# Performance work log

Hardware: AMD Instinct MI355X
Metric: run time of the kernel (lower is better)

The kernel has to match this reference:

```python
import jax, jax.numpy as jnp
import numpy as np

N, E, IN, H, D = 50000, 800000, 128, 2, 64  # heads=2, head_dim=64, hidden*2 = 128


def setup_inputs() -> dict:
    key = jax.random.key(0)
    ks = jax.random.split(key, 8)
    s = 1.0 / np.sqrt(IN)
    return {
        "x": jax.random.normal(ks[0], (N, IN), dtype=jnp.float32),
        "edge_index": jax.random.randint(ks[1], (2, E), 0, N, dtype=jnp.int64),
        "Wq": jax.random.normal(ks[2], (IN, H * D), dtype=jnp.float32) * s,
        "bq": jnp.zeros((H * D,), jnp.float32),
        "Wk": jax.random.normal(ks[3], (IN, H * D), dtype=jnp.float32) * s,
        "bk": jnp.zeros((H * D,), jnp.float32),
        "Wv": jax.random.normal(ks[4], (IN, H * D), dtype=jnp.float32) * s,
        "bv": jnp.zeros((H * D,), jnp.float32),
        "Wskip": jax.random.normal(ks[5], (IN, H * D), dtype=jnp.float32) * s,
        "bskip": jnp.zeros((H * D,), jnp.float32),
        "Wdec": jax.random.normal(ks[6], (H * D, IN), dtype=jnp.float32) * (1.0 / np.sqrt(H * D)),
        "bdec": jnp.zeros((IN,), jnp.float32),
    }


def reference(x, edge_index, Wq, bq, Wk, bk, Wv, bv, Wskip, bskip, Wdec, bdec):
    n = x.shape[0]
    src, dst = edge_index[0], edge_index[1]  # message flows src -> dst (PyG convention)
    q = (x @ Wq + bq).reshape(n, H, D)
    k = (x @ Wk + bk).reshape(n, H, D)
    v = (x @ Wv + bv).reshape(n, H, D)
    # per-edge multi-head scores [E, H]
    score = jnp.einsum('ehd,ehd->eh', q[dst], k[src]) / jnp.sqrt(jnp.asarray(D, x.dtype))
    # segment softmax over in-edges of each destination node
    m = jax.ops.segment_max(score, dst, num_segments=n)
    m = jnp.where(jnp.isfinite(m), m, jnp.zeros_like(m))  # nodes with no in-edges
    e = jnp.exp(score - m[dst])
    denom = jax.ops.segment_sum(e, dst, num_segments=n) + 1e-16
    alpha = e / denom[dst]                      # [E, H]
    msg = v[src] * alpha[..., None]             # [E, H, D]
    agg = jax.ops.segment_sum(msg, dst, num_segments=n)  # [N, H, D]
    z = agg.reshape(n, H * D) + (x @ Wskip + bskip)       # concat heads + root skip
    x_hat = z @ Wdec + bdec
    return (x_hat, z)
```

## Files before the change

### kernel.cpp

```cpp
#include <hip/hip_runtime.h>
#include <hip/hip_bf16.h>
#include <math.h>

typedef unsigned short u16;
typedef unsigned char u8;
typedef unsigned int u32;
typedef __attribute__((ext_vector_type(8))) short bf16x8;
typedef __attribute__((ext_vector_type(4))) float f32x4;

__device__ __forceinline__ float b2f(u16 u) {
  union { unsigned int i; float f; } x; x.i = ((unsigned int)u) << 16; return x.f;
}
__device__ __forceinline__ u16 f2b(float f) {
  union { float f; unsigned int i; } x; x.f = f;
  unsigned int r = x.i + 0x7FFFu + ((x.i >> 16) & 1u);
  return (u16)(r >> 16);
}
__device__ __forceinline__ float4 cvt4(ushort4 u) {
  return make_float4(b2f(u.x), b2f(u.y), b2f(u.z), b2f(u.w));
}
__device__ __forceinline__ float4 i8x4_to_f4(u32 w) {
  return make_float4((float)((int)(w << 24) >> 24), (float)((int)(w << 16) >> 24),
                     (float)((int)(w << 8) >> 24), (float)((int)w >> 24));
}

#if __has_builtin(__builtin_amdgcn_sdot4)
__device__ __forceinline__ int dot4i8(u32 a, u32 b) {
  return __builtin_amdgcn_sdot4((int)a, (int)b, 0, false);
}
#else
__device__ __forceinline__ int dot4i8(u32 a, u32 b) {
  int s = ((int)(a << 24) >> 24) * ((int)(b << 24) >> 24);
  s += ((int)(a << 16) >> 24) * ((int)(b << 16) >> 24);
  s += ((int)(a << 8) >> 24) * ((int)(b << 8) >> 24);
  s += ((int)a >> 24) * ((int)b >> 24);
  return s;
}
#endif

__device__ __forceinline__ bool ei_is_i64(const int* __restrict__ ei) {
  return (ei[1] | ei[3] | ei[5] | ei[7] | ei[9] | ei[11] | ei[13] | ei[15]) == 0;
}

__global__ __launch_bounds__(256) void prep_kernel(
    const float* __restrict__ Wq, const float* __restrict__ Wk,
    const float* __restrict__ Wv, const float* __restrict__ Wsk,
    const float* __restrict__ Wd,
    const float* __restrict__ bq, const float* __restrict__ bk,
    const float* __restrict__ bv, const float* __restrict__ bsk,
    const float* __restrict__ bd,
    short* __restrict__ Wt, float* __restrict__ bias,
    const int* __restrict__ ei, int* __restrict__ cnt,
    u8* __restrict__ rank, int E) {
  int g = blockIdx.x * 256 + threadIdx.x;
  if (g < 5 * 16384) {
    int mat = g >> 14, rem = g & 16383;
    int frag = rem >> 9;
    int l = (rem >> 3) & 63;
    int j = rem & 7;
    int nt = frag >> 2, s = frag & 3;
    int nrow = nt * 16 + (l & 15);
    int kcol = s * 32 + (l >> 4) * 8 + j;
    const float* W = (mat == 0) ? Wq : (mat == 1) ? Wk : (mat == 2) ? Wv
                     : (mat == 3) ? Wsk : Wd;
    float scl = (mat == 0) ? 0.125f : 1.f;
    Wt[g] = (short)f2b(W[kcol * 128 + nrow] * scl);
  }
  if (g < 5 * 128) {
    int mat = g >> 7, nn = g & 127;
    const float* B = (mat == 0) ? bq : (mat == 1) ? bk : (mat == 2) ? bv
                     : (mat == 3) ? bsk : bd;
    bias[g] = B[nn] * ((mat == 0) ? 0.125f : 1.f);
  }
  bool f = ei_is_i64(ei);
  if (g < E) {
    int idx = f ? (g << 1) : g;
    int dbase = f ? (E << 1) : E;
    int d = ei[dbase + idx];
    rank[g] = (u8)atomicAdd(&cnt[d], 1);
  }
}

__global__ __launch_bounds__(1024) void scanA_kernel(const int* __restrict__ cnt,
                                                     int* __restrict__ offs,
                                                     int* __restrict__ parts, int n) {
  __shared__ int wsum[16];
  int i = blockIdx.x * 1024 + threadIdx.x;
  int lane = threadIdx.x & 63, wid = threadIdx.x >> 6;
  int v = (i < n) ? cnt[i] : 0;
  int s = v;
#pragma unroll
  for (int off = 1; off < 64; off <<= 1) {
    int t = __shfl_up(s, off, 64);
    if (lane >= off) s += t;
  }
  if (lane == 63) wsum[wid] = s;
  __syncthreads();
  if (threadIdx.x == 0) {
    int acc = 0;
#pragma unroll
    for (int w = 0; w < 16; ++w) { int t = wsum[w]; wsum[w] = acc; acc += t; }
    parts[blockIdx.x] = acc;
  }
  __syncthreads();
  if (i < n) offs[i] = wsum[wid] + (s - v);
}

__global__ __launch_bounds__(1024) void scanC_kernel(int* __restrict__ offs,
                                                     const int* __restrict__ parts,
                                                     int n, int nb) {
  __shared__ int sh[2];
  if (threadIdx.x < 64) {
    int lane = threadIdx.x;
    int v = (lane < nb) ? parts[lane] : 0;
    int s = v;
#pragma unroll
    for (int off = 1; off < 64; off <<= 1) {
      int t = __shfl_up(s, off, 64);
      if (lane >= off) s += t;
    }
    int base = __shfl(s - v, blockIdx.x, 64);
    int tot  = __shfl(s, nb - 1, 64);
    if (lane == 0) { sh[0] = base; sh[1] = tot; }
  }
  __syncthreads();
  int i = blockIdx.x * 1024 + threadIdx.x;
  if (i < n) offs[i] += sh[0];
  if (i == 0) offs[n] = sh[1];
}

__global__ __launch_bounds__(512) void proj_kernel(const float* __restrict__ x,
    const short* __restrict__ Wt, const float* __restrict__ bias,
    u32* __restrict__ q8, float* __restrict__ qscb,
    u32* __restrict__ kvq, float* __restrict__ scb,
    u32* __restrict__ skip32, int n,
    const int* __restrict__ ei, const int* __restrict__ offs,
    const u8* __restrict__ rank, int* __restrict__ csr, int E) {
  __shared__ short xt[32 * 128];
  __shared__ u32 qsL[32 * 33];
  __shared__ u32 kvL[32 * 65];
  __shared__ u32 skL[32 * 65];
  __shared__ float qscL[32 * 2];
  __shared__ float scL[32 * 4];
  int m0 = blockIdx.x * 32;
  int tid = threadIdx.x;

  {
    int row = tid >> 4, c = tid & 15;
    int grow = m0 + row;
    bf16x8 val;
    if (grow < n) {
      const float* sp = x + (size_t)grow * 128 + c * 8;
      float4 f0 = *(const float4*)sp;
      float4 f1 = *(const float4*)(sp + 4);
      val[0] = (short)f2b(f0.x); val[1] = (short)f2b(f0.y);
      val[2] = (short)f2b(f0.z); val[3] = (short)f2b(f0.w);
      val[4] = (short)f2b(f1.x); val[5] = (short)f2b(f1.y);
      val[6] = (short)f2b(f1.z); val[7] = (short)f2b(f1.w);
    } else {
#pragma unroll
      for (int j = 0; j < 8; ++j) val[j] = 0;
    }
    *(bf16x8*)&xt[row * 128 + ((c ^ (row & 15)) << 3)] = val;
  }
  __syncthreads();

  int wid = tid >> 6, l = tid & 63;
  int mat = wid & 3, mhalf = wid >> 2;
  int lm = l & 15, lk = l >> 4;
  const short* Wl = Wt + (size_t)mat * 16384 + l * 8;
  int ml = mhalf * 16 + lm;
  f32x4 acc[8];
#pragma unroll
  for (int nt = 0; nt < 8; ++nt) acc[nt] = (f32x4){0.f, 0.f, 0.f, 0.f};

#pragma unroll
  for (int s = 0; s < 4; ++s) {
    int c = s * 4 + lk;
    bf16x8 bfrag = *(const bf16x8*)&xt[ml * 128 + ((c ^ (ml & 15)) << 3)];
#pragma unroll
    for (int nt = 0; nt < 8; ++nt) {
      bf16x8 afrag = *(const bf16x8*)(Wl + nt * 2048 + s * 512);
      acc[nt] = __builtin_amdgcn_mfma_f32_16x16x32_bf16(afrag, bfrag, acc[nt], 0, 0, 0);
    }
  }

  const float* bs = bias + mat * 128;
#pragma unroll
  for (int nt = 0; nt < 8; ++nt) {
    float4 b4 = *(const float4*)(bs + nt * 16 + lk * 4);
    acc[nt][0] += b4.x; acc[nt][1] += b4.y;
    acc[nt][2] += b4.z; acc[nt][3] += b4.w;
  }
  int lrow = mhalf * 16 + lm;
  if (mat < 3) {
#pragma unroll
    for (int h = 0; h < 2; ++h) {
      float am = 0.f;
#pragma unroll
      for (int nt4 = 0; nt4 < 4; ++nt4) {
        int nt = h * 4 + nt4;
#pragma unroll
        for (int j = 0; j < 4; ++j) am = fmaxf(am, fabsf(acc[nt][j]));
      }
      am = fmaxf(am, __shfl_xor(am, 16));
      am = fmaxf(am, __shfl_xor(am, 32));
      float inv = (am > 0.f) ? 127.f / am : 0.f;
#pragma unroll
      for (int nt4 = 0; nt4 < 4; ++nt4) {
        int nt = h * 4 + nt4;
        u32 pk = 0;
#pragma unroll
        for (int j = 0; j < 4; ++j) {
          float qv = fminf(fmaxf(rintf(acc[nt][j] * inv), -127.f), 127.f);
          pk |= ((u32)((int)qv & 0xff)) << (8 * j);
        }
        int slot = nt4 * 4 + lk;
        if (mat == 0) qsL[lrow * 33 + h * 16 + slot] = pk;
        else kvL[lrow * 65 + h * 32 + slot * 2 + (mat - 1)] = pk;
      }
      if (lk == 0) {
        float sc = am * (1.f / 127.f);
        if (mat == 0) qscL[lrow * 2 + h] = sc;
        else scL[lrow * 4 + h * 2 + (mat - 1)] = sc;
      }
    }
  } else {
#pragma unroll
    for (int nt = 0; nt < 8; ++nt) {
      u16 o0 = f2b(acc[nt][0]), o1 = f2b(acc[nt][1]);
      u16 o2 = f2b(acc[nt][2]), o3 = f2b(acc[nt][3]);
      int u = nt * 8 + lk * 2;
      skL[lrow * 65 + u]     = (u32)o0 | ((u32)o1 << 16);
      skL[lrow * 65 + u + 1] = (u32)o2 | ((u32)o3 << 16);
    }
  }
  __syncthreads();

  int nvalid = n - m0; if (nvalid > 32) nvalid = 32;
  for (int idx = tid; idx < nvalid * 32; idx += 512) {
    int node = idx >> 5, slot = idx & 31;
    q8[(size_t)(m0 + node) * 32 + slot] = qsL[node * 33 + slot];
  }
  for (int idx = tid; idx < nvalid * 64; idx += 512) {
    int node = idx >> 6, slot = idx & 63;
    kvq[(size_t)(m0 + node) * 64 + slot] = kvL[node * 65 + slot];
  }
  for (int idx = tid; idx < nvalid * 64; idx += 512) {
    int node = idx >> 6, slot = idx & 63;
    skip32[(size_t)(m0 + node) * 64 + slot] = skL[node * 65 + slot];
  }
  for (int idx = tid; idx < nvalid * 4; idx += 512) {
    int node = idx >> 2, s = idx & 3;
    scb[(size_t)(m0 + node) * 4 + s] = scL[node * 4 + s];
  }
  for (int idx = tid; idx < nvalid * 2; idx += 512) {
    int node = idx >> 1, h = idx & 1;
    qscb[(size_t)(m0 + node) * 2 + h] = qscL[node * 2 + h];
  }

  {
    bool f = ei_is_i64(ei);
    int stride = gridDim.x * 512;
    for (int e = blockIdx.x * 512 + tid; e < E; e += stride) {
      int idx = f ? (e << 1) : e;
      int dbase = f ? (E << 1) : E;
      int s = ei[idx];
      int d = ei[dbase + idx];
      int pos = offs[d] + (int)rank[e];
      __builtin_nontemporal_store(s, &csr[pos]);
    }
  }
}

__global__ __launch_bounds__(256) void dec_kernel(const float* __restrict__ zin,
    const short* __restrict__ Wt, const float* __restrict__ bias,
    float* __restrict__ out, int n) {
  __shared__ short zt[128 * 128];
  int m0 = blockIdx.x * 128;
  int tid = threadIdx.x;
#pragma unroll
  for (int p = 0; p < 8; ++p) {
    int cid = tid + p * 256;
    int row = cid >> 4, c = cid & 15;
    int grow = m0 + row;
    bf16x8 val;
    if (grow < n) {
      const float* sp = zin + (size_t)grow * 128 + c * 8;
      float4 f0 = *(const float4*)sp;
      float4 f1 = *(const float4*)(sp + 4);
      val[0] = (short)f2b(f0.x); val[1] = (short)f2b(f0.y);
      val[2] = (short)f2b(f0.z); val[3] = (short)f2b(f0.w);
      val[4] = (short)f2b(f1.x); val[5] = (short)f2b(f1.y);
      val[6] = (short)f2b(f1.z); val[7] = (short)f2b(f1.w);
    } else {
#pragma unroll
      for (int j = 0; j < 8; ++j) val[j] = 0;
    }
    *(bf16x8*)&zt[row * 128 + ((c ^ (row & 15)) << 3)] = val;
  }
  __syncthreads();

  int wid = tid >> 6, l = tid & 63;
  int lm = l & 15, lk = l >> 4;
  int mbase = wid * 32;
  const short* Wl = Wt + l * 8;
  f32x4 acc[2][8];
#pragma unroll
  for (int mt = 0; mt < 2; ++mt)
#pragma unroll
    for (int nt = 0; nt < 8; ++nt) acc[mt][nt] = (f32x4){0.f, 0.f, 0.f, 0.f};

#pragma unroll
  for (int s = 0; s < 4; ++s) {
    bf16x8 bfrag[2];
#pragma unroll
    for (int mt = 0; mt < 2; ++mt) {
      int ml = mbase + mt * 16 + lm;
      int c = s * 4 + lk;
      bfrag[mt] = *(const bf16x8*)&zt[ml * 128 + ((c ^ (ml & 15)) << 3)];
    }
#pragma unroll
    for (int nt = 0; nt < 8; ++nt) {
      bf16x8 afrag = *(const bf16x8*)(Wl + nt * 2048 + s * 512);
      acc[0][nt] = __builtin_amdgcn_mfma_f32_16x16x32_bf16(afrag, bfrag[0], acc[0][nt], 0, 0, 0);
      acc[1][nt] = __builtin_amdgcn_mfma_f32_16x16x32_bf16(afrag, bfrag[1], acc[1][nt], 0, 0, 0);
    }
  }

#pragma unroll
  for (int mt = 0; mt < 2; ++mt) {
    int m = m0 + mbase + mt * 16 + lm;
    if (m >= n) continue;
#pragma unroll
    for (int nt = 0; nt < 8; ++nt) {
      int n4 = nt * 16 + lk * 4;
      float4 b4 = *(const float4*)(bias + n4);
      f32x4 a = acc[mt][nt];
      *(float4*)(out + (size_t)m * 128 + n4) =
          make_float4(a[0] + b4.x, a[1] + b4.y, a[2] + b4.z, a[3] + b4.w);
    }
  }
}

#define PAIR_BODY(EA, EB, SACC, AACC, HM)                                    \
  {                                                                          \
    int e_ = half ? (EB) : (EA);                                             \
    u32 kvoff_ = (u32)e_ * 256u + (u32)(l32 * 8);                            \
    uint2 kv_ = *(const uint2*)(kvbytes + kvoff_);                           \
    float2 sc_ = *(const float2*)(scbytes + (u32)e_ * 16u + (u32)(h * 8));   \
    int pi_ = dot4i8(qw, kv_.x);                                             \
    pi_ += __shfl_xor(pi_, 1);                                               \
    pi_ += __shfl_xor(pi_, 2);                                               \
    pi_ += __shfl_xor(pi_, 4);                                               \
    pi_ += __shfl_xor(pi_, 8);                                               \
    float w_ = __expf((float)pi_ * (qs * sc_.x)) * (HM);                     \
    float4 vv_ = i8x4_to_f4(kv_.y);                                          \
    float wv_ = w_ * sc_.y;                                                  \
    SACC += w_;                                                              \
    AACC.x += wv_ * vv_.x; AACC.y += wv_ * vv_.y;                            \
    AACC.z += wv_ * vv_.z; AACC.w += wv_ * vv_.w;                            \
  }

__global__ __launch_bounds__(256) void attn_kernel(const u32* __restrict__ q8,
                                                   const float* __restrict__ qscb,
                                                   const u32* __restrict__ kvq,
                                                   const float* __restrict__ scb,
                                                   const u16* __restrict__ skipb,
                                                   const int* __restrict__ offs,
                                                   const int* __restrict__ csr,
                                                   float* __restrict__ z, int nn) {
  int wv = __builtin_amdgcn_readfirstlane((int)(threadIdx.x >> 6));
  int dst = blockIdx.x * 4 + wv;
  if (dst >= nn) return;
  int lane = threadIdx.x & 63;
  int half = lane >> 5;
  int l32 = lane & 31;
  int h = l32 >> 4;
  u32 qw = q8[(size_t)dst * 32 + l32];
  float qs = qscb[(size_t)dst * 2 + h];
  int i0 = __builtin_amdgcn_readfirstlane(offs[dst]);
  int i1 = __builtin_amdgcn_readfirstlane(offs[dst + 1]);
  const u8* kvbytes = (const u8*)kvq;
  const u8* scbytes = (const u8*)scb;
  float hm1 = (half == 0) ? 1.f : 0.f;

  float s0 = 0.f, s1 = 0.f, s2 = 0.f, s3 = 0.f;
  float4 A0 = {0, 0, 0, 0}, A1 = {0, 0, 0, 0}, A2 = {0, 0, 0, 0}, A3 = {0, 0, 0, 0};

  int i = i0;
  for (; i + 7 < i1; i += 8) {
    int e0 = csr[i], e1 = csr[i + 1], e2 = csr[i + 2], e3 = csr[i + 3];
    int e4 = csr[i + 4], e5 = csr[i + 5], e6 = csr[i + 6], e7 = csr[i + 7];
    PAIR_BODY(e0, e1, s0, A0, 1.f)
    PAIR_BODY(e2, e3, s1, A1, 1.f)
    PAIR_BODY(e4, e5, s2, A2, 1.f)
    PAIR_BODY(e6, e7, s3, A3, 1.f)
  }
  for (; i + 1 < i1; i += 2) {
    int e0 = csr[i], e1 = csr[i + 1];
    PAIR_BODY(e0, e1, s0, A0, 1.f)
  }
  if (i < i1) {
    int e0 = csr[i];
    PAIR_BODY(e0, e0, s0, A0, hm1)
  }

  float sum = (s0 + s1) + (s2 + s3);
  float b0 = (A0.x + A1.x) + (A2.x + A3.x);
  float b1 = (A0.y + A1.y) + (A2.y + A3.y);
  float b2 = (A0.z + A1.z) + (A2.z + A3.z);
  float b3 = (A0.w + A1.w) + (A2.w + A3.w);
  sum += __shfl_xor(sum, 32);
  b0 += __shfl_xor(b0, 32);
  b1 += __shfl_xor(b1, 32);
  b2 += __shfl_xor(b2, 32);
  b3 += __shfl_xor(b3, 32);
  if (half == 0) {
    float inv = 1.f / (sum + 1e-16f);
    int qoff = dst * 128 + h * 64 + (l32 & 15) * 4;
    float4 sk = cvt4(*(const ushort4*)(skipb + qoff));
    *(float4*)(z + qoff) = make_float4(b0 * inv + sk.x, b1 * inv + sk.y,
                                       b2 * inv + sk.z, b3 * inv + sk.w);
  }
}

extern "C" void kernel_launch(void* const* d_in, const int* in_sizes, int n_in,
                              void* d_out, int out_size, void* d_ws, size_t ws_size,
                              hipStream_t stream) {
  const float* x  = (const float*)d_in[0];
  const int*   ei = (const int*)d_in[1];
  const float* Wq = (const float*)d_in[2];
  const float* bq = (const float*)d_in[3];
  const float* Wk = (const float*)d_in[4];
  const float* bk = (const float*)d_in[5];
  const float* Wv = (const float*)d_in[6];
  const float* bv = (const float*)d_in[7];
  const float* Wsk = (const float*)d_in[8];
  const float* bsk = (const float*)d_in[9];
  const float* Wd = (const float*)d_in[10];
  const float* bd = (const float*)d_in[11];

  int N = in_sizes[0] / 128;
  int E = in_sizes[1] / 2;

  char* w = (char*)d_ws;
  auto alloc = [&](size_t bytes) {
    char* p = w;
    w += (bytes + 255) & ~(size_t)255;
    return p;
  };
  u32* q8    = (u32*)alloc((size_t)N * 32 * 4);
  float* qscb = (float*)alloc((size_t)N * 2 * 4);
  u32* kvq   = (u32*)alloc((size_t)N * 64 * 4);
  float* scb = (float*)alloc((size_t)N * 4 * 4);
  u16* skipb = (u16*)alloc((size_t)N * 128 * 2);
  int* cnt  = (int*)alloc((size_t)(N + 1) * 4);
  int* offs = (int*)alloc((size_t)(N + 1) * 4);
  u8*  rank = (u8*)alloc((size_t)E);
  int* csr  = (int*)alloc((size_t)E * 4);
  int* parts = (int*)alloc(66 * 4);
  short* Wt = (short*)alloc(5 * 16384 * 2);
  float* bias = (float*)alloc(5 * 128 * 4);

  float* xhat = (float*)d_out;
  float* z = xhat + (size_t)N * 128;

  int nb = (N + 1023) / 1024;
  int gp = (E + 255) / 256;
  if (gp < 320) gp = 320;

  hipMemsetAsync(cnt, 0, (size_t)N * 4, stream);
  prep_kernel<<<gp, 256, 0, stream>>>(Wq, Wk, Wv, Wsk, Wd, bq, bk, bv, bsk, bd,
                                      Wt, bias, ei, cnt, rank, E);
  scanA_kernel<<<nb, 1024, 0, stream>>>(cnt, offs, parts, N);
  scanC_kernel<<<nb, 1024, 0, stream>>>(offs, parts, N, nb);

  proj_kernel<<<(N + 31) / 32, 512, 0, stream>>>(x, Wt, bias, q8, qscb, kvq, scb,
                                                 (u32*)skipb, N, ei, offs, rank,
                                                 csr, E);

  attn_kernel<<<(N + 3) / 4, 256, 0, stream>>>(q8, qscb, kvq, scb, skipb, offs, csr,
                                               z, N);

  dec_kernel<<<(N + 127) / 128, 256, 0, stream>>>(z, Wt + 4 * 16384, bias + 4 * 128,
                                                  xhat, N);
}
```

Before: 156.9 us.

## Fuse attention aggregation and decoder GEMM into one kernel via shared-memory z tile

Merges the attention kernel and the decoder kernel. Each 512-thread block handles 128 destination nodes, 8 waves with 16 nodes each processed in turn, and writes z both to global memory and as bf16 into a swizzled LDS tile. The tile then feeds the MFMA decoder GEMM directly. This removes one launch and the decoder's re-read of z from global memory. In exchange the grid drops from about 12.5k blocks to about 391, each wave walks its nodes one after another, and the 32KB LDS tile limits occupancy, which reduces the latency hiding available to the gather-bound attention phase.

```diff
diff --git a/kernel.cpp b/kernel.cpp
--- a/kernel.cpp
+++ b/kernel.cpp
@@ -273,76 +273,6 @@
   }
 }
 
-__global__ __launch_bounds__(256) void dec_kernel(const float* __restrict__ zin,
-    const short* __restrict__ Wt, const float* __restrict__ bias,
-    float* __restrict__ out, int n) {
-  __shared__ short zt[128 * 128];
-  int m0 = blockIdx.x * 128;
-  int tid = threadIdx.x;
-#pragma unroll
-  for (int p = 0; p < 8; ++p) {
-    int cid = tid + p * 256;
-    int row = cid >> 4, c = cid & 15;
-    int grow = m0 + row;
-    bf16x8 val;
-    if (grow < n) {
-      const float* sp = zin + (size_t)grow * 128 + c * 8;
-      float4 f0 = *(const float4*)sp;
-      float4 f1 = *(const float4*)(sp + 4);
-      val[0] = (short)f2b(f0.x); val[1] = (short)f2b(f0.y);
-      val[2] = (short)f2b(f0.z); val[3] = (short)f2b(f0.w);
-      val[4] = (short)f2b(f1.x); val[5] = (short)f2b(f1.y);
-      val[6] = (short)f2b(f1.z); val[7] = (short)f2b(f1.w);
-    } else {
-#pragma unroll
-      for (int j = 0; j < 8; ++j) val[j] = 0;
-    }
-    *(bf16x8*)&zt[row * 128 + ((c ^ (row & 15)) << 3)] = val;
-  }
-  __syncthreads();
-
-  int wid = tid >> 6, l = tid & 63;
-  int lm = l & 15, lk = l >> 4;
-  int mbase = wid * 32;
-  const short* Wl = Wt + l * 8;
-  f32x4 acc[2][8];
-#pragma unroll
-  for (int mt = 0; mt < 2; ++mt)
-#pragma unroll
-    for (int nt = 0; nt < 8; ++nt) acc[mt][nt] = (f32x4){0.f, 0.f, 0.f, 0.f};
-
-#pragma unroll
-  for (int s = 0; s < 4; ++s) {
-    bf16x8 bfrag[2];
-#pragma unroll
-    for (int mt = 0; mt < 2; ++mt) {
-      int ml = mbase + mt * 16 + lm;
-      int c = s * 4 + lk;
-      bfrag[mt] = *(const bf16x8*)&zt[ml * 128 + ((c ^ (ml & 15)) << 3)];
-    }
-#pragma unroll
-    for (int nt = 0; nt < 8; ++nt) {
-      bf16x8 afrag = *(const bf16x8*)(Wl + nt * 2048 + s * 512);
-      acc[0][nt] = __builtin_amdgcn_mfma_f32_16x16x32_bf16(afrag, bfrag[0], acc[0][nt], 0, 0, 0);
-      acc[1][nt] = __builtin_amdgcn_mfma_f32_16x16x32_bf16(afrag, bfrag[1], acc[1][nt], 0, 0, 0);
-    }
-  }
-
-#pragma unroll
-  for (int mt = 0; mt < 2; ++mt) {
-    int m = m0 + mbase + mt * 16 + lm;
-    if (m >= n) continue;
-#pragma unroll
-    for (int nt = 0; nt < 8; ++nt) {
-      int n4 = nt * 16 + lk * 4;
-      float4 b4 = *(const float4*)(bias + n4);
-      f32x4 a = acc[mt][nt];
-      *(float4*)(out + (size_t)m * 128 + n4) =
-          make_float4(a[0] + b4.x, a[1] + b4.y, a[2] + b4.z, a[3] + b4.w);
-    }
-  }
-}
-
 #define PAIR_BODY(EA, EB, SACC, AACC, HM)                                    \
   {                                                                          \
     int e_ = half ? (EB) : (EA);                                             \
@@ -362,66 +292,109 @@
     AACC.z += wv_ * vv_.z; AACC.w += wv_ * vv_.w;                            \
   }
 
-__global__ __launch_bounds__(256) void attn_kernel(const u32* __restrict__ q8,
-                                                   const float* __restrict__ qscb,
-                                                   const u32* __restrict__ kvq,
-                                                   const float* __restrict__ scb,
-                                                   const u16* __restrict__ skipb,
-                                                   const int* __restrict__ offs,
-                                                   const int* __restrict__ csr,
-                                                   float* __restrict__ z, int nn) {
-  int wv = __builtin_amdgcn_readfirstlane((int)(threadIdx.x >> 6));
-  int dst = blockIdx.x * 4 + wv;
-  if (dst >= nn) return;
-  int lane = threadIdx.x & 63;
+__global__ __launch_bounds__(512) void attndec_kernel(const u32* __restrict__ q8,
+    const float* __restrict__ qscb, const u32* __restrict__ kvq,
+    const float* __restrict__ scb, const u16* __restrict__ skipb,
+    const int* __restrict__ offs, const int* __restrict__ csr,
+    const short* __restrict__ Wt, const float* __restrict__ bias,
+    float* __restrict__ z, float* __restrict__ xhat, int n) {
+  __shared__ short zt[128 * 128];
+  int m0 = blockIdx.x * 128;
+  int tid = threadIdx.x;
+  int wid = tid >> 6, lane = tid & 63;
   int half = lane >> 5;
   int l32 = lane & 31;
   int h = l32 >> 4;
-  u32 qw = q8[(size_t)dst * 32 + l32];
-  float qs = qscb[(size_t)dst * 2 + h];
-  int i0 = __builtin_amdgcn_readfirstlane(offs[dst]);
-  int i1 = __builtin_amdgcn_readfirstlane(offs[dst + 1]);
+  int l16 = l32 & 15;
   const u8* kvbytes = (const u8*)kvq;
   const u8* scbytes = (const u8*)scb;
   float hm1 = (half == 0) ? 1.f : 0.f;
 
-  float s0 = 0.f, s1 = 0.f, s2 = 0.f, s3 = 0.f;
-  float4 A0 = {0, 0, 0, 0}, A1 = {0, 0, 0, 0}, A2 = {0, 0, 0, 0}, A3 = {0, 0, 0, 0};
-
-  int i = i0;
-  for (; i + 7 < i1; i += 8) {
-    int e0 = csr[i], e1 = csr[i + 1], e2 = csr[i + 2], e3 = csr[i + 3];
-    int e4 = csr[i + 4], e5 = csr[i + 5], e6 = csr[i + 6], e7 = csr[i + 7];
-    PAIR_BODY(e0, e1, s0, A0, 1.f)
-    PAIR_BODY(e2, e3, s1, A1, 1.f)
-    PAIR_BODY(e4, e5, s2, A2, 1.f)
-    PAIR_BODY(e6, e7, s3, A3, 1.f)
-  }
-  for (; i + 1 < i1; i += 2) {
-    int e0 = csr[i], e1 = csr[i + 1];
-    PAIR_BODY(e0, e1, s0, A0, 1.f)
-  }
-  if (i < i1) {
-    int e0 = csr[i];
-    PAIR_BODY(e0, e0, s0, A0, hm1)
-  }
-
-  float sum = (s0 + s1) + (s2 + s3);
-  float b0 = (A0.x + A1.x) + (A2.x + A3.x);
-  float b1 = (A0.y + A1.y) + (A2.y + A3.y);
-  float b2 = (A0.z + A1.z) + (A2.z + A3.z);
-  float b3 = (A0.w + A1.w) + (A2.w + A3.w);
-  sum += __shfl_xor(sum, 32);
-  b0 += __shfl_xor(b0, 32);
-  b1 += __shfl_xor(b1, 32);
-  b2 += __shfl_xor(b2, 32);
-  b3 += __shfl_xor(b3, 32);
-  if (half == 0) {
-    float inv = 1.f / (sum + 1e-16f);
-    int qoff = dst * 128 + h * 64 + (l32 & 15) * 4;
-    float4 sk = cvt4(*(const ushort4*)(skipb + qoff));
-    *(float4*)(z + qoff) = make_float4(b0 * inv + sk.x, b1 * inv + sk.y,
-                                       b2 * inv + sk.z, b3 * inv + sk.w);
+  for (int t = 0; t < 16; ++t) {
+    int dst = m0 + wid * 16 + t;
+    if (dst >= n) break;
+    u32 qw = q8[(size_t)dst * 32 + l32];
+    float qs = qscb[(size_t)dst * 2 + h];
+    int i0 = __builtin_amdgcn_readfirstlane(offs[dst]);
+    int i1 = __builtin_amdgcn_readfirstlane(offs[dst + 1]);
+
+    float s0 = 0.f, s1 = 0.f, s2 = 0.f, s3 = 0.f;
+    float4 A0 = {0, 0, 0, 0}, A1 = {0, 0, 0, 0}, A2 = {0, 0, 0, 0}, A3 = {0, 0, 0, 0};
+
+    int i = i0;
+    for (; i + 7 < i1; i += 8) {
+      int e0 = csr[i], e1 = csr[i + 1], e2 = csr[i + 2], e3 = csr[i + 3];
+      int e4 = csr[i + 4], e5 = csr[i + 5], e6 = csr[i + 6], e7 = csr[i + 7];
+      PAIR_BODY(e0, e1, s0, A0, 1.f)
+      PAIR_BODY(e2, e3, s1, A1, 1.f)
+      PAIR_BODY(e4, e5, s2, A2, 1.f)
+      PAIR_BODY(e6, e7, s3, A3, 1.f)
+    }
+    for (; i + 1 < i1; i += 2) {
+      int e0 = csr[i], e1 = csr[i + 1];
+      PAIR_BODY(e0, e1, s0, A0, 1.f)
+    }
+    if (i < i1) {
+      int e0 = csr[i];
+      PAIR_BODY(e0, e0, s0, A0, hm1)
+    }
+
+    float sum = (s0 + s1) + (s2 + s3);
+    float b0 = (A0.x + A1.x) + (A2.x + A3.x);
+    float b1 = (A0.y + A1.y) + (A2.y + A3.y);
+    float b2 = (A0.z + A1.z) + (A2.z + A3.z);
+    float b3 = (A0.w + A1.w) + (A2.w + A3.w);
+    sum += __shfl_xor(sum, 32);
+    b0 += __shfl_xor(b0, 32);
+    b1 += __shfl_xor(b1, 32);
+    b2 += __shfl_xor(b2, 32);
+    b3 += __shfl_xor(b3, 32);
+    if (half == 0) {
+      float inv = 1.f / (sum + 1e-16f);
+      int d0 = h * 64 + l16 * 4;
+      int qoff = dst * 128 + d0;
+      float4 sk = cvt4(*(const ushort4*)(skipb + qoff));
+      float4 o = make_float4(b0 * inv + sk.x, b1 * inv + sk.y,
+                             b2 * inv + sk.z, b3 * inv + sk.w);
+      *(float4*)(z + qoff) = o;
+      int r = dst - m0;
+      int c = d0 >> 3;
+      ushort4 ob;
+      ob.x = f2b(o.x); ob.y = f2b(o.y); ob.z = f2b(o.z); ob.w = f2b(o.w);
+      *(ushort4*)&zt[r * 128 + ((c ^ (r & 15)) << 3) + (d0 & 7)] = ob;
+    }
+  }
+  __syncthreads();
+
+  int lm = lane & 15, lk = lane >> 4;
+  int mbase = wid * 16;
+  const short* Wl = Wt + lane * 8;
+  f32x4 acc[8];
+#pragma unroll
+  for (int nt = 0; nt < 8; ++nt) acc[nt] = (f32x4){0.f, 0.f, 0.f, 0.f};
+
+#pragma unroll
+  for (int s = 0; s < 4; ++s) {
+    int ml = mbase + lm;
+    int c = s * 4 + lk;
+    bf16x8 bfrag = *(const bf16x8*)&zt[ml * 128 + ((c ^ (ml & 15)) << 3)];
+#pragma unroll
+    for (int nt = 0; nt < 8; ++nt) {
+      bf16x8 afrag = *(const bf16x8*)(Wl + nt * 2048 + s * 512);
+      acc[nt] = __builtin_amdgcn_mfma_f32_16x16x32_bf16(afrag, bfrag, acc[nt], 0, 0, 0);
+    }
+  }
+
+  int m = m0 + mbase + lm;
+  if (m < n) {
+#pragma unroll
+    for (int nt = 0; nt < 8; ++nt) {
+      int n4 = nt * 16 + lk * 4;
+      float4 b4 = *(const float4*)(bias + n4);
+      f32x4 a = acc[nt];
+      *(float4*)(xhat + (size_t)m * 128 + n4) =
+          make_float4(a[0] + b4.x, a[1] + b4.y, a[2] + b4.z, a[3] + b4.w);
+    }
   }
 }
 
@@ -480,9 +453,7 @@
                                                  (u32*)skipb, N, ei, offs, rank,
                                                  csr, E);
 
-  attn_kernel<<<(N + 3) / 4, 256, 0, stream>>>(q8, qscb, kvq, scb, skipb, offs, csr,
-                                               z, N);
-
-  dec_kernel<<<(N + 127) / 128, 256, 0, stream>>>(z, Wt + 4 * 16384, bias + 4 * 128,
-                                                  xhat, N);
-}
+  attndec_kernel<<<(N + 127) / 128, 512, 0, stream>>>(q8, qscb, kvq, scb, skipb,
+                                                      offs, csr, Wt + 4 * 16384,
+                                                      bias + 4 * 128, z, xhat, N);
+}
```

Measured after the change: 174.3 us. 1.11x slower.
